# Kernel optimization log

Hardware: AMD Instinct MI355X
Metric: run time of the kernel (lower is better)

## Reference

```python
import jax, jax.numpy as jnp
import numpy as np

N = 50000      # nodes
E = 1600000    # edges (before self-loops)
H = 4          # heads
C = 32         # channels per head
HC = H * C     # hidden_channels = 128
IN = 128       # in_channels
NCLS = 4       # classifier out_channels
B = 512        # number of graphs
NEG_SLOPE = 0.2


def setup_inputs() -> dict:
    key = jax.random.key(0)
    ks = jax.random.split(key, 14)
    s = 0.1
    return {
        "x": jax.random.normal(ks[0], (N, IN), jnp.float32),
        "edge_index": jax.random.randint(ks[1], (2, E), 0, N, dtype=jnp.int32),
        "batch": jnp.sort(jax.random.randint(ks[2], (N,), 0, B, dtype=jnp.int32)),
        "w1": jax.random.normal(ks[3], (IN, HC), jnp.float32) * s,
        "as1": jax.random.normal(ks[4], (H, C), jnp.float32) * s,
        "ad1": jax.random.normal(ks[5], (H, C), jnp.float32) * s,
        "b1": jnp.zeros((HC,), jnp.float32),
        "w2": jax.random.normal(ks[6], (HC, HC), jnp.float32) * s,
        "as2": jax.random.normal(ks[7], (H, C), jnp.float32) * s,
        "ad2": jax.random.normal(ks[8], (H, C), jnp.float32) * s,
        "b2": jnp.zeros((HC,), jnp.float32),
        "wc": jax.random.normal(ks[9], (HC, NCLS), jnp.float32) * s,
        "bc": jnp.zeros((NCLS,), jnp.float32),
    }


def gat_conv(x, W, a_src, a_dst, bias, src, dst):
    # x: [N, F_in]; W: [F_in, H*C]
    h = (x @ W).reshape(N, H, C)                      # [N, H, C]
    e_src = jnp.einsum('nhc,hc->nh', h, a_src)        # [N, H]
    e_dst = jnp.einsum('nhc,hc->nh', h, a_dst)
    # per-edge attention logits, softmax grouped by destination node
    e = jax.nn.leaky_relu(e_src[src] + e_dst[dst], NEG_SLOPE)      # [E', H]
    m = jax.ops.segment_max(e, dst, num_segments=N)                # [N, H]
    m = jnp.where(jnp.isfinite(m), m, 0.0)
    ex = jnp.exp(e - jax.lax.stop_gradient(m)[dst])
    denom = jax.ops.segment_sum(ex, dst, num_segments=N)
    alpha = ex / (denom[dst] + 1e-16)                               # [E', H]
    out = jax.ops.segment_sum(alpha[:, :, None] * h[src], dst, num_segments=N)
    return out.reshape(N, HC) + bias                  # concat heads + bias


def reference(x, edge_index, batch, w1, as1, ad1, b1, w2, as2, ad2, b2, wc, bc):
    x = x.astype(jnp.float32)
    # GATConv default add_self_loops=True
    loops = jnp.arange(N, dtype=edge_index.dtype)
    src = jnp.concatenate([edge_index[0], loops])
    dst = jnp.concatenate([edge_index[1], loops])
    h = gat_conv(x, w1, as1, ad1, b1, src, dst)
    h = jax.nn.relu(h)                                # act between layers; dropout=0 (eval)
    h = gat_conv(h, w2, as2, ad2, b2, src, dst)
    # global_mean_pool over batch ids
    sums = jax.ops.segment_sum(h, batch, num_segments=B)            # [B, HC]
    cnts = jax.ops.segment_sum(jnp.ones((N,), h.dtype), batch, num_segments=B)
    pooled = sums / jnp.maximum(cnts, 1.0)[:, None]
    return pooled @ wc + bc                            # [B, NCLS]
```

## Files before the change

### kernel.cpp

```cpp
#include <hip/hip_runtime.h>
#include <hip/hip_fp16.h>

#define N_NODES 50000
#define N_EDGES 1600000
#define EPLUS   1650000
#define HCH 128
#define NB 512
#define NCLS 4
#define NBUCK 782
#define NSB 256
#define PCHUNK 6446

typedef unsigned int uint;

__device__ __forceinline__ float lrelu(float v) { return v > 0.f ? v : 0.2f * v; }

__device__ __forceinline__ float fdot2(uint a, uint b, float c) {
  asm("v_dot2_f32_f16 %0, %1, %2, %0" : "+v"(c) : "v"(a), "v"(b));
  return c;
}

__device__ __forceinline__ uint pkrtz(float a, float b) {
  auto v = __builtin_amdgcn_cvt_pkrtz(a, b);
  uint r;
  __builtin_memcpy(&r, &v, 4);
  return r;
}

__device__ __forceinline__ uint pkrn(float a, float b) {
  return (uint)__half_as_ushort(__float2half_rn(a)) |
         ((uint)__half_as_ushort(__float2half_rn(b)) << 16);
}

__global__ __launch_bounds__(256) void k_pA(const int* __restrict__ ei,
                                            int* __restrict__ M) {
  __shared__ int lh[NBUCK];
  for (int k = threadIdx.x; k < NBUCK; k += 256) lh[k] = 0;
  __syncthreads();
  int lo = blockIdx.x * PCHUNK;
  int hi = lo + PCHUNK; if (hi > EPLUS) hi = EPLUS;
  for (int e = lo + threadIdx.x; e < hi; e += 256) {
    int dst = (e < N_EDGES) ? ei[N_EDGES + e] : (e - N_EDGES);
    atomicAdd(&lh[dst >> 6], 1);
  }
  __syncthreads();
  for (int k = threadIdx.x; k < NBUCK; k += 256)
    M[blockIdx.x * NBUCK + k] = lh[k];
}

__global__ __launch_bounds__(256) void k_pB1(int* __restrict__ M,
                                             int* __restrict__ tot) {
  __shared__ int sm[256];
  int k = blockIdx.x;
  int t = threadIdx.x;
  int v = M[t * NBUCK + k];
  sm[t] = v;
  __syncthreads();
  for (int off = 1; off < 256; off <<= 1) {
    int u = (t >= off) ? sm[t - off] : 0;
    __syncthreads();
    sm[t] += u;
    __syncthreads();
  }
  M[t * NBUCK + k] = sm[t] - v;
  if (t == 255) tot[k] = sm[255];
}

__global__ __launch_bounds__(1024) void k_pB2(const int* __restrict__ tot,
                                              int* __restrict__ bucketstart) {
  __shared__ int sm[1024];
  int k = threadIdx.x;
  int v = (k < NBUCK) ? tot[k] : 0;
  sm[k] = v;
  __syncthreads();
  for (int off = 1; off < 1024; off <<= 1) {
    int u = (k >= off) ? sm[k - off] : 0;
    __syncthreads();
    sm[k] += u;
    __syncthreads();
  }
  if (k < NBUCK) {
    bucketstart[k] = sm[k] - v;
    if (k == NBUCK - 1) bucketstart[NBUCK] = sm[k];
  }
}

__global__ __launch_bounds__(256) void k_pC(const int* __restrict__ ei,
                                            const int* __restrict__ M,
                                            const int* __restrict__ bucketstart,
                                            uint* __restrict__ part) {
  __shared__ int lbase[NBUCK];
  __shared__ int lc[NBUCK];
  for (int k = threadIdx.x; k < NBUCK; k += 256) {
    lbase[k] = bucketstart[k] + M[blockIdx.x * NBUCK + k];
    lc[k] = 0;
  }
  __syncthreads();
  int lo = blockIdx.x * PCHUNK;
  int hi = lo + PCHUNK; if (hi > EPLUS) hi = EPLUS;
  for (int e = lo + threadIdx.x; e < hi; e += 256) {
    int src, dst;
    if (e < N_EDGES) { src = ei[e]; dst = ei[N_EDGES + e]; }
    else { src = dst = e - N_EDGES; }
    int b = dst >> 6;
    int p = lbase[b] + atomicAdd(&lc[b], 1);
    part[p] = (uint)src | ((uint)dst << 16);
  }
}

__global__ __launch_bounds__(256) void k_pD(const uint* __restrict__ part,
                                            const int* __restrict__ bucketstart,
                                            int* __restrict__ rowstart,
                                            int* __restrict__ col) {
  __shared__ int dcnt[64], dstart[64], dc2[64];
  int b = blockIdx.x;
  int n0 = bucketstart[b], n1 = bucketstart[b + 1];
  int t = threadIdx.x;
  if (t < 64) { dcnt[t] = 0; dc2[t] = 0; }
  __syncthreads();
  for (int i = n0 + t; i < n1; i += 256)
    atomicAdd(&dcnt[(part[i] >> 16) & 63], 1);
  __syncthreads();
  if (t < 64) {
    int v = dcnt[t];
    int run = v;
    #pragma unroll
    for (int off = 1; off < 64; off <<= 1) {
      int u = __shfl_up(run, off);
      if (t >= off) run += u;
    }
    dstart[t] = run - v;
    int node = b * 64 + t;
    if (node < N_NODES) rowstart[node] = n0 + run - v;
  }
  if (b == NBUCK - 1 && t == 0) rowstart[N_NODES] = n1;
  __syncthreads();
  for (int i = n0 + t; i < n1; i += 256) {
    uint pr = part[i];
    int loc = (pr >> 16) & 63;
    int pos = n0 + dstart[loc] + atomicAdd(&dc2[loc], 1);
    col[pos] = (int)(pr & 0xffffu);
  }
}

template<int XF16>
__global__ __launch_bounds__(256) void k_gemm_fused(const float* __restrict__ X,
                                                    const uint* __restrict__ X16,
                                                    const float* __restrict__ W,
                                                    const float* __restrict__ asrc,
                                                    const float* __restrict__ adst,
                                                    uint* __restrict__ hbu,
                                                    float* __restrict__ es,
                                                    float* __restrict__ ed) {
  __shared__ uint As16[64][20];
  __shared__ uint Bs2[128][18];
  int tid = threadIdx.x;
  int r0 = blockIdx.x * 64;
  int tm = tid >> 4;
  int tn = tid & 15;
  float acc[4][8];
  #pragma unroll
  for (int i = 0; i < 4; ++i)
    #pragma unroll
    for (int j = 0; j < 8; ++j) acc[i][j] = 0.f;

  for (int kc = 0; kc < 128; kc += 32) {
    if (XF16) {
      int row = tid >> 2;
      int kq4 = (tid & 3) * 4;
      int gr = r0 + row;
      uint4 v = make_uint4(0u, 0u, 0u, 0u);
      if (gr < N_NODES) v = *(const uint4*)&X16[(size_t)gr * 64 + (kc >> 1) + kq4];
      *(uint4*)&As16[row][kq4] = v;
    } else {
      #pragma unroll
      for (int i = 0; i < 2; ++i) {
        int q = tid + 256 * i;
        int row = q >> 3;
        int kq = (q & 7) << 2;
        int gr = r0 + row;
        float4 v = make_float4(0.f, 0.f, 0.f, 0.f);
        if (gr < N_NODES) v = *(const float4*)&X[(size_t)gr * 128 + kc + kq];
        As16[row][(kq >> 1) + 0] = pkrn(v.x, v.y);
        As16[row][(kq >> 1) + 1] = pkrn(v.z, v.w);
      }
    }
    {
      int kk = tid >> 4;
      int c8 = (tid & 15) * 8;
      const float* wr0 = &W[(size_t)(kc + 2 * kk) * 128 + c8];
      float4 w0a = *(const float4*)wr0;
      float4 w0b = *(const float4*)(wr0 + 4);
      float4 w1a = *(const float4*)(wr0 + 128);
      float4 w1b = *(const float4*)(wr0 + 132);
      float w0v[8] = {w0a.x, w0a.y, w0a.z, w0a.w, w0b.x, w0b.y, w0b.z, w0b.w};
      float w1v[8] = {w1a.x, w1a.y, w1a.z, w1a.w, w1b.x, w1b.y, w1b.z, w1b.w};
      #pragma unroll
      for (int j = 0; j < 8; ++j)
        Bs2[j * 16 + (tid & 15)][kk] = pkrn(w0v[j], w1v[j]);
    }
    __syncthreads();
    #pragma unroll
    for (int kk = 0; kk < 16; kk += 2) {
      uint2 a0 = *(const uint2*)&As16[tm +  0][kk];
      uint2 a1 = *(const uint2*)&As16[tm + 16][kk];
      uint2 a2 = *(const uint2*)&As16[tm + 32][kk];
      uint2 a3 = *(const uint2*)&As16[tm + 48][kk];
      #pragma unroll
      for (int j = 0; j < 8; ++j) {
        uint2 b = *(const uint2*)&Bs2[j * 16 + tn][kk];
        acc[0][j] = fdot2(a0.x, b.x, acc[0][j]);
        acc[0][j] = fdot2(a0.y, b.y, acc[0][j]);
        acc[1][j] = fdot2(a1.x, b.x, acc[1][j]);
        acc[1][j] = fdot2(a1.y, b.y, acc[1][j]);
        acc[2][j] = fdot2(a2.x, b.x, acc[2][j]);
        acc[2][j] = fdot2(a2.y, b.y, acc[2][j]);
        acc[3][j] = fdot2(a3.x, b.x, acc[3][j]);
        acc[3][j] = fdot2(a3.y, b.y, acc[3][j]);
      }
    }
    __syncthreads();
  }

  float av_s[8], av_d[8];
  #pragma unroll
  for (int j = 0; j < 8; ++j) { av_s[j] = asrc[tn * 8 + j]; av_d[j] = adst[tn * 8 + j]; }
  int head = tn >> 2;
  #pragma unroll
  for (int i = 0; i < 4; ++i) {
    int row = r0 + tm + 16 * i;
    float ps = 0.f, pd = 0.f;
    uint us[8];
    #pragma unroll
    for (int j = 0; j < 8; ++j) {
      float v = acc[i][j];
      ps = fmaf(v, av_s[j], ps);
      pd = fmaf(v, av_d[j], pd);
      us[j] = (uint)__half_as_ushort(__float2half_rn(v));
    }
    ps += __shfl_xor(ps, 1); ps += __shfl_xor(ps, 2);
    pd += __shfl_xor(pd, 1); pd += __shfl_xor(pd, 2);
    if (row < N_NODES) {
      uint4 p;
      p.x = us[0] | (us[1] << 16);
      p.y = us[2] | (us[3] << 16);
      p.z = us[4] | (us[5] << 16);
      p.w = us[6] | (us[7] << 16);
      *(uint4*)&hbu[(size_t)row * 64 + tn * 4] = p;
      if ((tn & 3) == 0) {
        es[row * 4 + head] = ps;
        ed[row * 4 + head] = pd;
      }
    }
  }
}

__global__ __launch_bounds__(256) void k_attn(const uint* __restrict__ hb,
                                              const float* __restrict__ es,
                                              const float* __restrict__ ed,
                                              const int* __restrict__ rowstart,
                                              const int* __restrict__ col,
                                              const float* __restrict__ bias,
                                              float* __restrict__ outp,
                                              uint* __restrict__ out16,
                                              int do_relu, int wf16) {
  __shared__ float swv[4][4 * 68];
  __shared__ int   ssc[4][64];
  int lane = threadIdx.x & 63;
  int wv = threadIdx.x >> 6;
  int n = blockIdx.x * 4 + wv;
  if (n >= N_NODES) return;
  int s = rowstart[n], t = rowstart[n + 1];
  int sub = lane & 15;
  int esel = lane >> 4;
  int head2 = sub >> 2;
  float4 edv = *(const float4*)&ed[n * 4];
  const char* hbb = (const char*)hb + (uint)sub * 16u;
  const char* esb = (const char*)es;
  float* wv0 = swv[wv];
  int* sc0 = ssc[wv];

  float4 denv = make_float4(0.f, 0.f, 0.f, 0.f);
  float acc[8];
  #pragma unroll
  for (int j = 0; j < 8; ++j) acc[j] = 0.f;

  for (int base = s; base < t; base += 64) {
    int nthis = t - base; if (nthis > 64) nthis = 64;
    int npad = (nthis + 15) & ~15;
    if (lane < nthis) {
      int sc = col[base + lane];
      float4 esv = *(const float4*)(esb + ((uint)sc << 4));
      float w0 = __expf(lrelu(esv.x + edv.x));
      float w1 = __expf(lrelu(esv.y + edv.y));
      float w2 = __expf(lrelu(esv.z + edv.z));
      float w3 = __expf(lrelu(esv.w + edv.w));
      denv.x += w0; denv.y += w1; denv.z += w2; denv.w += w3;
      wv0[0 * 68 + lane] = w0;
      wv0[1 * 68 + lane] = w1;
      wv0[2 * 68 + lane] = w2;
      wv0[3 * 68 + lane] = w3;
      sc0[lane] = sc << 8;
    } else if (lane < npad) {
      wv0[0 * 68 + lane] = 0.f;
      wv0[1 * 68 + lane] = 0.f;
      wv0[2 * 68 + lane] = 0.f;
      wv0[3 * 68 + lane] = 0.f;
      sc0[lane] = 0;
    }
    asm volatile("s_waitcnt lgkmcnt(0)" ::: "memory");
    __builtin_amdgcn_s_setprio(1);
    for (int i = 0; i < npad; i += 16) {
      int e0 = i + esel, e1 = e0 + 4, e2 = e0 + 8, e3 = e0 + 12;
      float w0 = wv0[head2 * 68 + e0];
      float w1 = wv0[head2 * 68 + e1];
      float w2 = wv0[head2 * 68 + e2];
      float w3 = wv0[head2 * 68 + e3];
      int so0 = sc0[e0], so1 = sc0[e1], so2 = sc0[e2], so3 = sc0[e3];
      uint4 q0 = *(const uint4*)(hbb + (uint)so0);
      uint4 q1 = *(const uint4*)(hbb + (uint)so1);
      uint4 q2 = *(const uint4*)(hbb + (uint)so2);
      uint4 q3 = *(const uint4*)(hbb + (uint)so3);
      uint wa = pkrtz(w0, w1);
      uint wb = pkrtz(w2, w3);
      acc[0] = fdot2(__builtin_amdgcn_perm(q1.x, q0.x, 0x05040100u), wa, acc[0]);
      acc[1] = fdot2(__builtin_amdgcn_perm(q1.x, q0.x, 0x07060302u), wa, acc[1]);
      acc[2] = fdot2(__builtin_amdgcn_perm(q1.y, q0.y, 0x05040100u), wa, acc[2]);
      acc[3] = fdot2(__builtin_amdgcn_perm(q1.y, q0.y, 0x07060302u), wa, acc[3]);
      acc[4] = fdot2(__builtin_amdgcn_perm(q1.z, q0.z, 0x05040100u), wa, acc[4]);
      acc[5] = fdot2(__builtin_amdgcn_perm(q1.z, q0.z, 0x07060302u), wa, acc[5]);
      acc[6] = fdot2(__builtin_amdgcn_perm(q1.w, q0.w, 0x05040100u), wa, acc[6]);
      acc[7] = fdot2(__builtin_amdgcn_perm(q1.w, q0.w, 0x07060302u), wa, acc[7]);
      acc[0] = fdot2(__builtin_amdgcn_perm(q3.x, q2.x, 0x05040100u), wb, acc[0]);
      acc[1] = fdot2(__builtin_amdgcn_perm(q3.x, q2.x, 0x07060302u), wb, acc[1]);
      acc[2] = fdot2(__builtin_amdgcn_perm(q3.y, q2.y, 0x05040100u), wb, acc[2]);
      acc[3] = fdot2(__builtin_amdgcn_perm(q3.y, q2.y, 0x07060302u), wb, acc[3]);
      acc[4] = fdot2(__builtin_amdgcn_perm(q3.z, q2.z, 0x05040100u), wb, acc[4]);
      acc[5] = fdot2(__builtin_amdgcn_perm(q3.z, q2.z, 0x07060302u), wb, acc[5]);
      acc[6] = fdot2(__builtin_amdgcn_perm(q3.w, q2.w, 0x05040100u), wb, acc[6]);
      acc[7] = fdot2(__builtin_amdgcn_perm(q3.w, q2.w, 0x07060302u), wb, acc[7]);
    }
    __builtin_amdgcn_s_setprio(0);
  }
  #pragma unroll
  for (int j = 0; j < 8; ++j) {
    acc[j] += __shfl_xor(acc[j], 16);
    acc[j] += __shfl_xor(acc[j], 32);
  }
  #pragma unroll
  for (int off = 1; off < 64; off <<= 1) {
    denv.x += __shfl_xor(denv.x, off);
    denv.y += __shfl_xor(denv.y, off);
    denv.z += __shfl_xor(denv.z, off);
    denv.w += __shfl_xor(denv.w, off);
  }
  float den = (head2 & 2) ? ((head2 & 1) ? denv.w : denv.z)
                          : ((head2 & 1) ? denv.y : denv.x);
  float inv = 1.0f / (den + 1e-16f);
  if (lane < 32) {
    int half = lane >> 4;
    int c = sub * 8 + half * 4;
    float4 bb = *(const float4*)&bias[c];
    float o0 = acc[half * 4 + 0] * inv + bb.x;
    float o1 = acc[half * 4 + 1] * inv + bb.y;
    float o2 = acc[half * 4 + 2] * inv + bb.z;
    float o3 = acc[half * 4 + 3] * inv + bb.w;
    if (do_relu) {
      o0 = fmaxf(o0, 0.f); o1 = fmaxf(o1, 0.f);
      o2 = fmaxf(o2, 0.f); o3 = fmaxf(o3, 0.f);
    }
    if (wf16) {
      uint2 p2;
      p2.x = pkrn(o0, o1);
      p2.y = pkrn(o2, o3);
      *(uint2*)&out16[(size_t)n * 64 + sub * 4 + half * 2] = p2;
    } else {
      *(float4*)&outp[(size_t)n * 128 + c] = make_float4(o0, o1, o2, o3);
    }
  }
}

__global__ __launch_bounds__(128) void k_poolcls(const float* __restrict__ out2,
                                                 const int* __restrict__ batch,
                                                 const float* __restrict__ wc,
                                                 const float* __restrict__ bc,
                                                 float* __restrict__ y) {
  int b = blockIdx.x;
  int c = threadIdx.x;
  int lo = 0, hi = N_NODES;
  while (lo < hi) { int mid = (lo + hi) >> 1; if (batch[mid] < b) lo = mid + 1; else hi = mid; }
  int s = lo;
  lo = s; hi = N_NODES;
  while (lo < hi) { int mid = (lo + hi) >> 1; if (batch[mid] < b + 1) lo = mid + 1; else hi = mid; }
  int e = lo;
  float acc0 = 0.f, acc1 = 0.f, acc2 = 0.f, acc3 = 0.f;
  int nidx = s;
  for (; nidx + 4 <= e; nidx += 4) {
    acc0 += out2[(size_t)nidx * 128 + c];
    acc1 += out2[(size_t)(nidx + 1) * 128 + c];
    acc2 += out2[(size_t)(nidx + 2) * 128 + c];
    acc3 += out2[(size_t)(nidx + 3) * 128 + c];
  }
  for (; nidx < e; ++nidx) acc0 += out2[(size_t)nidx * 128 + c];
  float acc = (acc0 + acc1) + (acc2 + acc3);
  float cnt = (float)(e - s);
  float pooled = acc / fmaxf(cnt, 1.0f);
  float4 wrow = *(const float4*)&wc[c * 4];
  float wj[4] = {wrow.x, wrow.y, wrow.z, wrow.w};
  __shared__ float red[128];
  #pragma unroll
  for (int j = 0; j < 4; ++j) {
    red[c] = pooled * wj[j];
    __syncthreads();
    for (int off = 64; off > 0; off >>= 1) {
      if (c < off) red[c] += red[c + off];
      __syncthreads();
    }
    if (c == 0) y[b * 4 + j] = red[0] + bc[j];
    __syncthreads();
  }
}

extern "C" void kernel_launch(void* const* d_in, const int* in_sizes, int n_in,
                              void* d_out, int out_size, void* d_ws, size_t ws_size,
                              hipStream_t stream) {
  const float* x    = (const float*)d_in[0];
  const int*   ei   = (const int*)d_in[1];
  const int*   batch= (const int*)d_in[2];
  const float* w1   = (const float*)d_in[3];
  const float* as1  = (const float*)d_in[4];
  const float* ad1  = (const float*)d_in[5];
  const float* b1   = (const float*)d_in[6];
  const float* w2   = (const float*)d_in[7];
  const float* as2  = (const float*)d_in[8];
  const float* ad2  = (const float*)d_in[9];
  const float* b2   = (const float*)d_in[10];
  const float* wc   = (const float*)d_in[11];
  const float* bc   = (const float*)d_in[12];
  float* y = (float*)d_out;

  char* ws = (char*)d_ws;
  size_t o = 0;
  auto take = [&](size_t bytes) { void* p = ws + o; o = (o + bytes + 255) & ~(size_t)255; return p; };
  uint*  hbu      = (uint*)take((size_t)N_NODES * 64 * 4);
  uint*  h1u      = (uint*)take((size_t)N_NODES * 64 * 4);
  float* obuf     = (float*)take((size_t)N_NODES * HCH * 4);
  float* es       = (float*)take((size_t)N_NODES * 4 * 4);
  float* ed       = (float*)take((size_t)N_NODES * 4 * 4);
  int*   M        = (int*)take((size_t)NSB * NBUCK * 4);
  int*   tot      = (int*)take((size_t)NBUCK * 4);
  int*   bstart   = (int*)take((size_t)(NBUCK + 1) * 4);
  uint*  part     = (uint*)take((size_t)EPLUS * 4);
  int*   rowstart = (int*)take((size_t)(N_NODES + 1) * 4);
  int*   col      = (int*)take((size_t)EPLUS * 4);

  const int GW = N_NODES / 4;
  const int GG = (N_NODES + 63) / 64;

  k_pA<<<NSB, 256, 0, stream>>>(ei, M);
  k_pB1<<<NBUCK, 256, 0, stream>>>(M, tot);
  k_pB2<<<1, 1024, 0, stream>>>(tot, bstart);
  k_pC<<<NSB, 256, 0, stream>>>(ei, M, bstart, part);
  k_pD<<<NBUCK, 256, 0, stream>>>(part, bstart, rowstart, col);

  k_gemm_fused<0><<<GG, 256, 0, stream>>>(x, nullptr, w1, as1, ad1, hbu, es, ed);
  k_attn<<<GW, 256, 0, stream>>>(hbu, es, ed, rowstart, col, b1, obuf, h1u, 1, 1);

  k_gemm_fused<1><<<GG, 256, 0, stream>>>(nullptr, h1u, w2, as2, ad2, hbu, es, ed);
  k_attn<<<GW, 256, 0, stream>>>(hbu, es, ed, rowstart, col, b2, obuf, h1u, 0, 0);

  k_poolcls<<<NB, 128, 0, stream>>>(obuf, batch, wc, bc, y);
}
```

Measured before the change: 235.1 us.

## Use MFMA f16 matrix instructions for fused node GEMM

Replaces the v_dot2-based scalar GEMM in the fused projection kernel with MFMA 16x16x32 f16 instructions. The full K=128 tile of X and W is loaded into shared memory at once instead of in four K chunks, which removes the per-chunk barriers. The epilogue is rewritten for the MFMA output layout, using cross-lane shuffles for the attention dot products and for packing the f16 output. The output stores become 4-byte scattered writes instead of 16-byte vector stores, and shared memory use grows.

```diff
diff --git a/kernel.cpp b/kernel.cpp
--- a/kernel.cpp
+++ b/kernel.cpp
@@ -12,6 +12,8 @@
 #define PCHUNK 6446
 
 typedef unsigned int uint;
+typedef __attribute__((ext_vector_type(8))) _Float16 f16x8;
+typedef __attribute__((ext_vector_type(4))) float f32x4;
 
 __device__ __forceinline__ float lrelu(float v) { return v > 0.f ? v : 0.2f * v; }
 
@@ -152,104 +154,104 @@
                                                     uint* __restrict__ hbu,
                                                     float* __restrict__ es,
                                                     float* __restrict__ ed) {
-  __shared__ uint As16[64][20];
-  __shared__ uint Bs2[128][18];
+  __shared__ uint As[64][68];
+  __shared__ uint Bf[32 * 256];
   int tid = threadIdx.x;
+  int lane = tid & 63;
+  int wv = tid >> 6;
   int r0 = blockIdx.x * 64;
-  int tm = tid >> 4;
-  int tn = tid & 15;
-  float acc[4][8];
-  #pragma unroll
-  for (int i = 0; i < 4; ++i)
-    #pragma unroll
-    for (int j = 0; j < 8; ++j) acc[i][j] = 0.f;
-
-  for (int kc = 0; kc < 128; kc += 32) {
-    if (XF16) {
-      int row = tid >> 2;
-      int kq4 = (tid & 3) * 4;
+
+  if (XF16) {
+    #pragma unroll
+    for (int i = 0; i < 4; ++i) {
+      int q = tid + 256 * i;
+      int row = q >> 4;
+      int u4 = q & 15;
       int gr = r0 + row;
       uint4 v = make_uint4(0u, 0u, 0u, 0u);
-      if (gr < N_NODES) v = *(const uint4*)&X16[(size_t)gr * 64 + (kc >> 1) + kq4];
-      *(uint4*)&As16[row][kq4] = v;
-    } else {
+      if (gr < N_NODES) v = *(const uint4*)&X16[(size_t)gr * 64 + u4 * 4];
+      *(uint4*)&As[row][u4 * 4] = v;
+    }
+  } else {
+    #pragma unroll
+    for (int i = 0; i < 8; ++i) {
+      int q = tid + 256 * i;
+      int row = q >> 5;
+      int f4 = q & 31;
+      int gr = r0 + row;
+      float4 v = make_float4(0.f, 0.f, 0.f, 0.f);
+      if (gr < N_NODES) v = *(const float4*)&X[(size_t)gr * 128 + f4 * 4];
+      As[row][f4 * 2 + 0] = pkrn(v.x, v.y);
+      As[row][f4 * 2 + 1] = pkrn(v.z, v.w);
+    }
+  }
+  #pragma unroll
+  for (int i = 0; i < 8; ++i) {
+    int f = wv + 4 * i;
+    int t = f >> 2, kb = f & 3;
+    int c = t * 16 + (lane & 15);
+    int k0 = kb * 32 + (lane >> 4) * 8;
+    const float* wp = &W[(size_t)k0 * 128 + c];
+    uint4 b;
+    b.x = pkrn(wp[0],   wp[128]);
+    b.y = pkrn(wp[256], wp[384]);
+    b.z = pkrn(wp[512], wp[640]);
+    b.w = pkrn(wp[768], wp[896]);
+    *(uint4*)&Bf[f * 256 + lane * 4] = b;
+  }
+  __syncthreads();
+
+  int rb = wv * 16;
+  f32x4 acc[8];
+  #pragma unroll
+  for (int t = 0; t < 8; ++t) acc[t] = (f32x4){0.f, 0.f, 0.f, 0.f};
+  #pragma unroll
+  for (int kb = 0; kb < 4; ++kb) {
+    uint4 a4 = *(const uint4*)&As[rb + (lane & 15)][kb * 16 + (lane >> 4) * 4];
+    f16x8 af; __builtin_memcpy(&af, &a4, 16);
+    #pragma unroll
+    for (int t = 0; t < 8; ++t) {
+      uint4 b4 = *(const uint4*)&Bf[(t * 4 + kb) * 256 + lane * 4];
+      f16x8 bfr; __builtin_memcpy(&bfr, &b4, 16);
+      acc[t] = __builtin_amdgcn_mfma_f32_16x16x32_f16(af, bfr, acc[t], 0, 0, 0);
+    }
+  }
+
+  float asv[8], adv[8];
+  #pragma unroll
+  for (int t = 0; t < 8; ++t) {
+    asv[t] = asrc[t * 16 + (lane & 15)];
+    adv[t] = adst[t * 16 + (lane & 15)];
+  }
+  #pragma unroll
+  for (int j = 0; j < 4; ++j) {
+    int row = r0 + rb + (lane >> 4) * 4 + j;
+    float ps[4], pd[4];
+    #pragma unroll
+    for (int m = 0; m < 4; ++m) {
+      ps[m] = fmaf(acc[2 * m][j], asv[2 * m], acc[2 * m + 1][j] * asv[2 * m + 1]);
+      pd[m] = fmaf(acc[2 * m][j], adv[2 * m], acc[2 * m + 1][j] * adv[2 * m + 1]);
+    }
+    #pragma unroll
+    for (int off = 1; off < 16; off <<= 1) {
       #pragma unroll
-      for (int i = 0; i < 2; ++i) {
-        int q = tid + 256 * i;
-        int row = q >> 3;
-        int kq = (q & 7) << 2;
-        int gr = r0 + row;
-        float4 v = make_float4(0.f, 0.f, 0.f, 0.f);
-        if (gr < N_NODES) v = *(const float4*)&X[(size_t)gr * 128 + kc + kq];
-        As16[row][(kq >> 1) + 0] = pkrn(v.x, v.y);
-        As16[row][(kq >> 1) + 1] = pkrn(v.z, v.w);
+      for (int m = 0; m < 4; ++m) {
+        ps[m] += __shfl_xor(ps[m], off);
+        pd[m] += __shfl_xor(pd[m], off);
       }
     }
-    {
-      int kk = tid >> 4;
-      int c8 = (tid & 15) * 8;
-      const float* wr0 = &W[(size_t)(kc + 2 * kk) * 128 + c8];
-      float4 w0a = *(const float4*)wr0;
-      float4 w0b = *(const float4*)(wr0 + 4);
-      float4 w1a = *(const float4*)(wr0 + 128);
-      float4 w1b = *(const float4*)(wr0 + 132);
-      float w0v[8] = {w0a.x, w0a.y, w0a.z, w0a.w, w0b.x, w0b.y, w0b.z, w0b.w};
-      float w1v[8] = {w1a.x, w1a.y, w1a.z, w1a.w, w1b.x, w1b.y, w1b.z, w1b.w};
+    #pragma unroll
+    for (int t = 0; t < 8; ++t) {
+      float other = __shfl_xor(acc[t][j], 1);
+      if (!(lane & 1) && row < N_NODES) {
+        hbu[(size_t)row * 64 + t * 8 + ((lane & 15) >> 1)] = pkrn(acc[t][j], other);
+      }
+    }
+    if ((lane & 15) == 0 && row < N_NODES) {
       #pragma unroll
-      for (int j = 0; j < 8; ++j)
-        Bs2[j * 16 + (tid & 15)][kk] = pkrn(w0v[j], w1v[j]);
-    }
-    __syncthreads();
-    #pragma unroll
-    for (int kk = 0; kk < 16; kk += 2) {
-      uint2 a0 = *(const uint2*)&As16[tm +  0][kk];
-      uint2 a1 = *(const uint2*)&As16[tm + 16][kk];
-      uint2 a2 = *(const uint2*)&As16[tm + 32][kk];
-      uint2 a3 = *(const uint2*)&As16[tm + 48][kk];
-      #pragma unroll
-      for (int j = 0; j < 8; ++j) {
-        uint2 b = *(const uint2*)&Bs2[j * 16 + tn][kk];
-        acc[0][j] = fdot2(a0.x, b.x, acc[0][j]);
-        acc[0][j] = fdot2(a0.y, b.y, acc[0][j]);
-        acc[1][j] = fdot2(a1.x, b.x, acc[1][j]);
-        acc[1][j] = fdot2(a1.y, b.y, acc[1][j]);
-        acc[2][j] = fdot2(a2.x, b.x, acc[2][j]);
-        acc[2][j] = fdot2(a2.y, b.y, acc[2][j]);
-        acc[3][j] = fdot2(a3.x, b.x, acc[3][j]);
-        acc[3][j] = fdot2(a3.y, b.y, acc[3][j]);
-      }
-    }
-    __syncthreads();
-  }
-
-  float av_s[8], av_d[8];
-  #pragma unroll
-  for (int j = 0; j < 8; ++j) { av_s[j] = asrc[tn * 8 + j]; av_d[j] = adst[tn * 8 + j]; }
-  int head = tn >> 2;
-  #pragma unroll
-  for (int i = 0; i < 4; ++i) {
-    int row = r0 + tm + 16 * i;
-    float ps = 0.f, pd = 0.f;
-    uint us[8];
-    #pragma unroll
-    for (int j = 0; j < 8; ++j) {
-      float v = acc[i][j];
-      ps = fmaf(v, av_s[j], ps);
-      pd = fmaf(v, av_d[j], pd);
-      us[j] = (uint)__half_as_ushort(__float2half_rn(v));
-    }
-    ps += __shfl_xor(ps, 1); ps += __shfl_xor(ps, 2);
-    pd += __shfl_xor(pd, 1); pd += __shfl_xor(pd, 2);
-    if (row < N_NODES) {
-      uint4 p;
-      p.x = us[0] | (us[1] << 16);
-      p.y = us[2] | (us[3] << 16);
-      p.z = us[4] | (us[5] << 16);
-      p.w = us[6] | (us[7] << 16);
-      *(uint4*)&hbu[(size_t)row * 64 + tn * 4] = p;
-      if ((tn & 3) == 0) {
-        es[row * 4 + head] = ps;
-        ed[row * 4 + head] = pd;
+      for (int m = 0; m < 4; ++m) {
+        es[row * 4 + m] = ps[m];
+        ed[row * 4 + m] = pd[m];
       }
     }
   }
```

Result: faster. 218.8 us (-6.9%).
